# Kernel optimization log

Hardware: AMD Instinct MI355X
Metric: run time of the kernel (lower is better)

Reference implementation:

```python
import jax, jax.numpy as jnp
import numpy as np
from functools import partial

NUM_STEPS = 30  # Euler integration steps (inte_steps)


def _point_sample(vol, pts):
    """Trilinear sample of vol [C,D,H,W] at pts [N,3] (voxel coords, (d,h,w) order).
    Matches torch grid_sample(mode='bilinear', padding_mode='border', align_corners=True)
    after the normalize+flip done in PointPooling. Returns [C,N]."""
    dims = jnp.asarray(vol.shape[1:], dtype=pts.dtype)  # (D,H,W)
    p = jnp.clip(pts, 0.0, dims - 1.0)  # border padding == clamp coords
    p0 = jnp.floor(p)
    frac = p - p0  # [N,3]
    i0 = p0.astype(jnp.int32)
    i1 = jnp.minimum(i0 + 1, (dims - 1.0).astype(jnp.int32))
    d0, h0, w0 = i0[:, 0], i0[:, 1], i0[:, 2]
    d1, h1, w1 = i1[:, 0], i1[:, 1], i1[:, 2]
    fd, fh, fw = frac[:, 0], frac[:, 1], frac[:, 2]
    g = lambda d, h, w: vol[:, d, h, w]  # [C,N] gather
    c000, c001 = g(d0, h0, w0), g(d0, h0, w1)
    c010, c011 = g(d0, h1, w0), g(d0, h1, w1)
    c100, c101 = g(d1, h0, w0), g(d1, h0, w1)
    c110, c111 = g(d1, h1, w0), g(d1, h1, w1)
    c00 = c000 * (1 - fw) + c001 * fw
    c01 = c010 * (1 - fw) + c011 * fw
    c10 = c100 * (1 - fw) + c101 * fw
    c11 = c110 * (1 - fw) + c111 * fw
    c0 = c00 * (1 - fh) + c01 * fh
    c1 = c10 * (1 - fh) + c11 * fh
    return c0 * (1 - fd) + c1 * fd  # [C,N]


def _interp(flow, x):
    # flow [B,3,D,H,W], x [B,N,3] -> [B,N,3]
    out = jax.vmap(_point_sample)(flow, x)  # [B,3,N]
    return jnp.transpose(out, (0, 2, 1))


def _integrate_euler(flow, x, num_steps):
    flow = flow * (1.0 / num_steps)
    def step(x, _):
        return x + _interp(flow, x), None
    x, _ = jax.lax.scan(step, x, None, length=num_steps)
    return x


def _forward(verts, affine, flow_field):
    B, N, _ = verts.shape
    ones = jnp.ones((B, N, 1), dtype=verts.dtype)
    homog = jnp.concatenate([verts, ones], axis=-1)  # [B,N,4]
    pred = jnp.einsum('bij,bnj->bni', affine, homog)[..., :3]
    aux = _integrate_euler(flow_field, pred, NUM_STEPS)
    flow_int = aux - pred  # [B,N,3]
    pred = aux
    flow_int = jnp.transpose(flow_int, (0, 2, 1))[..., None, None]  # [B,3,N,1,1]
    homog2 = jnp.concatenate([pred, ones], axis=-1)
    inv_aff = jnp.linalg.inv(affine)
    pred = jnp.einsum('bij,bnj->bni', inv_aff, homog2)[..., :3]
    return pred, flow_int


def setup_inputs() -> dict:
    key = jax.random.key(0)
    k1, k2, k3 = jax.random.split(key, 3)
    B, N = 2, 140000
    D = H = W = 192
    dims = jnp.asarray([D - 1, H - 1, W - 1], dtype=jnp.float32)
    verts = jax.random.uniform(k1, (B, N, 3), dtype=jnp.float32) * dims
    affine = jnp.eye(4, dtype=jnp.float32)[None] + 0.01 * jax.random.normal(k2, (B, 4, 4), dtype=jnp.float32)
    flow_field = jax.random.normal(k3, (B, 3, D, H, W), dtype=jnp.float32)
    return {"verts": verts, "affine": affine, "flow_field": flow_field}


def reference(verts, affine, flow_field):
    return _forward(verts, affine, flow_field)
```

## Files before the change

### kernel.cpp

```cpp
#include <hip/hip_runtime.h>

#define NSTEPS 30
#define DIM 192
static constexpr int DHW = DIM * DIM * DIM;
static constexpr int PTS_PER_WAVE = 21;

__global__ void invert4x4_kernel(const float* __restrict__ aff,
                                 float* __restrict__ out, int B) {
    int b = blockIdx.x * blockDim.x + threadIdx.x;
    if (b >= B) return;
    double a[16];
#pragma unroll
    for (int i = 0; i < 16; i++) a[i] = (double)aff[b * 16 + i];

    double s0 = a[0]*a[5]  - a[4]*a[1];
    double s1 = a[0]*a[6]  - a[4]*a[2];
    double s2 = a[0]*a[7]  - a[4]*a[3];
    double s3 = a[1]*a[6]  - a[5]*a[2];
    double s4 = a[1]*a[7]  - a[5]*a[3];
    double s5 = a[2]*a[7]  - a[6]*a[3];
    double c5 = a[10]*a[15] - a[14]*a[11];
    double c4 = a[9]*a[15]  - a[13]*a[11];
    double c3 = a[9]*a[14]  - a[13]*a[10];
    double c2 = a[8]*a[15]  - a[12]*a[11];
    double c1 = a[8]*a[14]  - a[12]*a[10];
    double c0 = a[8]*a[13]  - a[12]*a[9];
    double det = s0*c5 - s1*c4 + s2*c3 + s3*c2 - s4*c1 + s5*c0;
    double inv = 1.0 / det;

    double o[16];
    o[0]  = ( a[5]*c5 - a[6]*c4 + a[7]*c3) * inv;
    o[1]  = (-a[1]*c5 + a[2]*c4 - a[3]*c3) * inv;
    o[2]  = ( a[13]*s5 - a[14]*s4 + a[15]*s3) * inv;
    o[3]  = (-a[9]*s5 + a[10]*s4 - a[11]*s3) * inv;
    o[4]  = (-a[4]*c5 + a[6]*c2 - a[7]*c1) * inv;
    o[5]  = ( a[0]*c5 - a[2]*c2 + a[3]*c1) * inv;
    o[6]  = (-a[12]*s5 + a[14]*s2 - a[15]*s1) * inv;
    o[7]  = ( a[8]*s5 - a[10]*s2 + a[11]*s1) * inv;
    o[8]  = ( a[4]*c4 - a[5]*c2 + a[7]*c0) * inv;
    o[9]  = (-a[0]*c4 + a[1]*c2 - a[3]*c0) * inv;
    o[10] = ( a[12]*s4 - a[13]*s2 + a[15]*s0) * inv;
    o[11] = (-a[8]*s4 + a[9]*s2 - a[11]*s0) * inv;
    o[12] = (-a[4]*c3 + a[5]*c1 - a[6]*c0) * inv;
    o[13] = ( a[0]*c3 - a[1]*c1 + a[2]*c0) * inv;
    o[14] = (-a[12]*s3 + a[13]*s1 - a[14]*s0) * inv;
    o[15] = ( a[8]*s3 - a[9]*s1 + a[10]*s0) * inv;
#pragma unroll
    for (int i = 0; i < 16; i++) out[b * 16 + i] = (float)o[i];
}

__global__ __launch_bounds__(256) void deform_kernel(
    const float* __restrict__ verts,
    const float* __restrict__ affine,
    const float* __restrict__ flow,
    const float* __restrict__ invaff,
    float* __restrict__ out_pred,
    float* __restrict__ out_flow,
    int N, int B) {
    int lane = threadIdx.x & 63;
    int wib  = threadIdx.x >> 6;
    long gwave = (long)blockIdx.x * (blockDim.x >> 6) + wib;

    int piw = lane / 3;
    if (piw > PTS_PER_WAVE - 1) piw = PTS_PER_WAVE - 1;
    int ch = lane - piw * 3;
    if (ch > 2) ch = 2;

    long pt = gwave * PTS_PER_WAVE + piw;
    bool valid = (lane < 63) && (pt < (long)B * N);
    long ptc = valid ? pt : ((long)B * N - 1);
    int b = (int)(ptc / N);
    int n = (int)(ptc - (long)b * N);

    const float* A = affine + b * 16;
    const float* v = verts + (size_t)ptc * 3;
    float vx = v[0], vy = v[1], vz = v[2];
    float x = A[0] * vx + A[1] * vy + A[2]  * vz + A[3];
    float y = A[4] * vx + A[5] * vy + A[6]  * vz + A[7];
    float z = A[8] * vx + A[9] * vy + A[10] * vz + A[11];
    float p0 = (ch == 0) ? x : (ch == 1) ? y : z;

    const float* Fc = flow + ((size_t)b * 3 + ch) * (size_t)DHW;
    const float scale = (float)(1.0 / NSTEPS);

    float cc[8];
    int key = -1;
    int bl = piw * 3;

    for (int s = 0; s < NSTEPS; s++) {
        float pd = fminf(fmaxf(x, 0.0f), (float)(DIM - 1));
        float ph = fminf(fmaxf(y, 0.0f), (float)(DIM - 1));
        float pw = fminf(fmaxf(z, 0.0f), (float)(DIM - 1));
        float fd0 = floorf(pd), fh0 = floorf(ph), fw0 = floorf(pw);
        int d0 = (int)fd0, h0 = (int)fh0, w0 = (int)fw0;
        float fd = pd - fd0, fh = ph - fh0, fw = pw - fw0;

        int k = (d0 * DIM + h0) * DIM + w0;
        if (k != key) {
            key = k;
            int d1 = min(d0 + 1, DIM - 1);
            int h1 = min(h0 + 1, DIM - 1);
            int w1 = min(w0 + 1, DIM - 1);
            int r00 = (d0 * DIM + h0) * DIM;
            int r01 = (d0 * DIM + h1) * DIM;
            int r10 = (d1 * DIM + h0) * DIM;
            int r11 = (d1 * DIM + h1) * DIM;
            cc[0] = Fc[r00 + w0] * scale;
            cc[1] = Fc[r00 + w1] * scale;
            cc[2] = Fc[r01 + w0] * scale;
            cc[3] = Fc[r01 + w1] * scale;
            cc[4] = Fc[r10 + w0] * scale;
            cc[5] = Fc[r10 + w1] * scale;
            cc[6] = Fc[r11 + w0] * scale;
            cc[7] = Fc[r11 + w1] * scale;
        }

        float omfw = 1.0f - fw, omfh = 1.0f - fh, omfd = 1.0f - fd;
        float c00 = cc[0] * omfw + cc[1] * fw;
        float c01 = cc[2] * omfw + cc[3] * fw;
        float c10 = cc[4] * omfw + cc[5] * fw;
        float c11 = cc[6] * omfw + cc[7] * fw;
        float c0 = c00 * omfh + c01 * fh;
        float c1 = c10 * omfh + c11 * fh;
        float val = c0 * omfd + c1 * fd;

        float v0 = __shfl(val, bl,     64);
        float v1 = __shfl(val, bl + 1, 64);
        float v2 = __shfl(val, bl + 2, 64);
        x += v0; y += v1; z += v2;
    }

    if (valid) {
        float posc = (ch == 0) ? x : (ch == 1) ? y : z;
        float fint = posc - p0;
        const float* Ai = invaff + b * 16 + ch * 4;
        float o = Ai[0] * x + Ai[1] * y + Ai[2] * z + Ai[3];
        out_pred[(size_t)ptc * 3 + ch] = o;
        out_flow[(size_t)b * 3 * N + (size_t)ch * N + n] = fint;
    }
}

extern "C" void kernel_launch(void* const* d_in, const int* in_sizes, int n_in,
                              void* d_out, int out_size, void* d_ws, size_t ws_size,
                              hipStream_t stream) {
    const float* verts  = (const float*)d_in[0];
    const float* affine = (const float*)d_in[1];
    const float* flow   = (const float*)d_in[2];

    int B = in_sizes[1] / 16;
    int N = in_sizes[0] / (3 * B);

    float* invaff   = (float*)d_ws;
    float* out_pred = (float*)d_out;
    float* out_flow = out_pred + (size_t)B * N * 3;

    hipLaunchKernelGGL(invert4x4_kernel, dim3(1), dim3(64), 0, stream,
                       affine, invaff, B);

    long total_pts = (long)B * N;
    long waves  = (total_pts + PTS_PER_WAVE - 1) / PTS_PER_WAVE;
    long blocks = (waves + 3) / 4;
    hipLaunchKernelGGL(deform_kernel, dim3((unsigned)blocks), dim3(256), 0, stream,
                       verts, affine, flow, invaff, out_pred, out_flow, N, B);
}
```

Baseline: 316.6 us.

## Repack flow field into interleaved fp16 channels before Euler integration

Result: faster. 306.1 us (-3.3%).

```diff
diff --git a/kernel.cpp b/kernel.cpp
--- a/kernel.cpp
+++ b/kernel.cpp
@@ -1,8 +1,9 @@
 #include <hip/hip_runtime.h>
+#include <hip/hip_fp16.h>
 
 #define NSTEPS 30
 #define DIM 192
-static constexpr int DHW = DIM * DIM * DIM;
+static constexpr long DHW = (long)DIM * DIM * DIM;
 static constexpr int PTS_PER_WAVE = 21;
 
 __global__ void invert4x4_kernel(const float* __restrict__ aff,
@@ -12,7 +13,6 @@
     double a[16];
 #pragma unroll
     for (int i = 0; i < 16; i++) a[i] = (double)aff[b * 16 + i];
-
     double s0 = a[0]*a[5]  - a[4]*a[1];
     double s1 = a[0]*a[6]  - a[4]*a[2];
     double s2 = a[0]*a[7]  - a[4]*a[3];
@@ -27,7 +27,6 @@
     double c0 = a[8]*a[13]  - a[12]*a[9];
     double det = s0*c5 - s1*c4 + s2*c3 + s3*c2 - s4*c1 + s5*c0;
     double inv = 1.0 / det;
-
     double o[16];
     o[0]  = ( a[5]*c5 - a[6]*c4 + a[7]*c3) * inv;
     o[1]  = (-a[1]*c5 + a[2]*c4 - a[3]*c3) * inv;
@@ -49,6 +48,113 @@
     for (int i = 0; i < 16; i++) out[b * 16 + i] = (float)o[i];
 }
 
+__global__ __launch_bounds__(256) void repack_kernel(const float* __restrict__ flow,
+                                                     __half* __restrict__ packed) {
+    long vox = (long)blockIdx.x * blockDim.x + threadIdx.x;
+    int b = blockIdx.y;
+    if (vox >= DHW) return;
+    const float* F = flow + (size_t)b * 3 * DHW;
+    float f0 = F[vox];
+    float f1 = F[vox + DHW];
+    float f2 = F[vox + 2 * DHW];
+    union { __half2 h2[2]; int2 i2; } u;
+    u.h2[0] = __floats2half2_rn(f0, f1);
+    u.h2[1] = __floats2half2_rn(f2, 0.0f);
+    reinterpret_cast<int2*>(packed)[(size_t)b * DHW + vox] = u.i2;
+}
+
+__global__ __launch_bounds__(256) void deform_packed_kernel(
+    const float* __restrict__ verts,
+    const float* __restrict__ affine,
+    const __half* __restrict__ packed,
+    const float* __restrict__ invaff,
+    float* __restrict__ out_pred,
+    float* __restrict__ out_flow,
+    int N, int B) {
+    int lane = threadIdx.x & 63;
+    int wib  = threadIdx.x >> 6;
+    long gwave = (long)blockIdx.x * (blockDim.x >> 6) + wib;
+
+    int piw = lane / 3;
+    if (piw > PTS_PER_WAVE - 1) piw = PTS_PER_WAVE - 1;
+    int ch = lane - piw * 3;
+    if (ch > 2) ch = 2;
+
+    long pt = gwave * PTS_PER_WAVE + piw;
+    bool valid = (lane < 63) && (pt < (long)B * N);
+    long ptc = valid ? pt : ((long)B * N - 1);
+    int b = (int)(ptc / N);
+    int n = (int)(ptc - (long)b * N);
+
+    const float* A = affine + b * 16;
+    const float* v = verts + (size_t)ptc * 3;
+    float vx = v[0], vy = v[1], vz = v[2];
+    float x = A[0] * vx + A[1] * vy + A[2]  * vz + A[3];
+    float y = A[4] * vx + A[5] * vy + A[6]  * vz + A[7];
+    float z = A[8] * vx + A[9] * vy + A[10] * vz + A[11];
+    float p0 = (ch == 0) ? x : (ch == 1) ? y : z;
+
+    const __half* Pb = packed + ((size_t)b * DHW) * 4 + ch;
+    const float scale = (float)(1.0 / NSTEPS);
+
+    float cc[8];
+    int key = -1;
+    int bl = piw * 3;
+
+    for (int s = 0; s < NSTEPS; s++) {
+        float pd = fminf(fmaxf(x, 0.0f), (float)(DIM - 1));
+        float ph = fminf(fmaxf(y, 0.0f), (float)(DIM - 1));
+        float pw = fminf(fmaxf(z, 0.0f), (float)(DIM - 1));
+        float fd0 = floorf(pd), fh0 = floorf(ph), fw0 = floorf(pw);
+        int d0 = (int)fd0, h0 = (int)fh0, w0 = (int)fw0;
+        float fd = pd - fd0, fh = ph - fh0, fw = pw - fw0;
+
+        int k = (d0 * DIM + h0) * DIM + w0;
+        if (k != key) {
+            key = k;
+            int d1 = min(d0 + 1, DIM - 1);
+            int h1 = min(h0 + 1, DIM - 1);
+            int w1 = min(w0 + 1, DIM - 1);
+            size_t r00 = (size_t)((d0 * DIM + h0) * DIM) * 4;
+            size_t r01 = (size_t)((d0 * DIM + h1) * DIM) * 4;
+            size_t r10 = (size_t)((d1 * DIM + h0) * DIM) * 4;
+            size_t r11 = (size_t)((d1 * DIM + h1) * DIM) * 4;
+            size_t o0 = (size_t)w0 * 4, o1 = (size_t)w1 * 4;
+            cc[0] = __half2float(Pb[r00 + o0]) * scale;
+            cc[1] = __half2float(Pb[r00 + o1]) * scale;
+            cc[2] = __half2float(Pb[r01 + o0]) * scale;
+            cc[3] = __half2float(Pb[r01 + o1]) * scale;
+            cc[4] = __half2float(Pb[r10 + o0]) * scale;
+            cc[5] = __half2float(Pb[r10 + o1]) * scale;
+            cc[6] = __half2float(Pb[r11 + o0]) * scale;
+            cc[7] = __half2float(Pb[r11 + o1]) * scale;
+        }
+
+        float omfw = 1.0f - fw, omfh = 1.0f - fh, omfd = 1.0f - fd;
+        float c00 = cc[0] * omfw + cc[1] * fw;
+        float c01 = cc[2] * omfw + cc[3] * fw;
+        float c10 = cc[4] * omfw + cc[5] * fw;
+        float c11 = cc[6] * omfw + cc[7] * fw;
+        float c0 = c00 * omfh + c01 * fh;
+        float c1 = c10 * omfh + c11 * fh;
+        float val = c0 * omfd + c1 * fd;
+
+        float v0 = __shfl(val, bl,     64);
+        float v1 = __shfl(val, bl + 1, 64);
+        float v2 = __shfl(val, bl + 2, 64);
+        x += v0; y += v1; z += v2;
+    }
+
+    if (valid) {
+        float posc = (ch == 0) ? x : (ch == 1) ? y : z;
+        float fint = posc - p0;
+        const float* Ai = invaff + b * 16 + ch * 4;
+        float o = Ai[0] * x + Ai[1] * y + Ai[2] * z + Ai[3];
+        out_pred[(size_t)ptc * 3 + ch] = o;
+        out_flow[(size_t)b * 3 * N + (size_t)ch * N + n] = fint;
+    }
+}
+
 __global__ __launch_bounds__(256) void deform_kernel(
     const float* __restrict__ verts,
     const float* __restrict__ affine,
@@ -60,18 +166,15 @@
     int lane = threadIdx.x & 63;
     int wib  = threadIdx.x >> 6;
     long gwave = (long)blockIdx.x * (blockDim.x >> 6) + wib;
-
     int piw = lane / 3;
     if (piw > PTS_PER_WAVE - 1) piw = PTS_PER_WAVE - 1;
     int ch = lane - piw * 3;
     if (ch > 2) ch = 2;
-
     long pt = gwave * PTS_PER_WAVE + piw;
     bool valid = (lane < 63) && (pt < (long)B * N);
     long ptc = valid ? pt : ((long)B * N - 1);
     int b = (int)(ptc / N);
     int n = (int)(ptc - (long)b * N);
-
     const float* A = affine + b * 16;
     const float* v = verts + (size_t)ptc * 3;
     float vx = v[0], vy = v[1], vz = v[2];
@@ -79,14 +182,11 @@
     float y = A[4] * vx + A[5] * vy + A[6]  * vz + A[7];
     float z = A[8] * vx + A[9] * vy + A[10] * vz + A[11];
     float p0 = (ch == 0) ? x : (ch == 1) ? y : z;
-
     const float* Fc = flow + ((size_t)b * 3 + ch) * (size_t)DHW;
     const float scale = (float)(1.0 / NSTEPS);
-
     float cc[8];
     int key = -1;
     int bl = piw * 3;
-
     for (int s = 0; s < NSTEPS; s++) {
         float pd = fminf(fmaxf(x, 0.0f), (float)(DIM - 1));
         float ph = fminf(fmaxf(y, 0.0f), (float)(DIM - 1));
@@ -94,7 +194,6 @@
         float fd0 = floorf(pd), fh0 = floorf(ph), fw0 = floorf(pw);
         int d0 = (int)fd0, h0 = (int)fh0, w0 = (int)fw0;
         float fd = pd - fd0, fh = ph - fh0, fw = pw - fw0;
-
         int k = (d0 * DIM + h0) * DIM + w0;
         if (k != key) {
             key = k;
@@ -114,7 +213,6 @@
             cc[6] = Fc[r11 + w0] * scale;
             cc[7] = Fc[r11 + w1] * scale;
         }
-
         float omfw = 1.0f - fw, omfh = 1.0f - fh, omfd = 1.0f - fd;
         float c00 = cc[0] * omfw + cc[1] * fw;
         float c01 = cc[2] * omfw + cc[3] * fw;
@@ -123,13 +221,11 @@
         float c0 = c00 * omfh + c01 * fh;
         float c1 = c10 * omfh + c11 * fh;
         float val = c0 * omfd + c1 * fd;
-
         float v0 = __shfl(val, bl,     64);
         float v1 = __shfl(val, bl + 1, 64);
         float v2 = __shfl(val, bl + 2, 64);
         x += v0; y += v1; z += v2;
     }
-
     if (valid) {
         float posc = (ch == 0) ? x : (ch == 1) ? y : z;
         float fint = posc - p0;
@@ -150,16 +246,33 @@
     int B = in_sizes[1] / 16;
     int N = in_sizes[0] / (3 * B);
 
-    float* invaff   = (float*)d_ws;
     float* out_pred = (float*)d_out;
     float* out_flow = out_pred + (size_t)B * N * 3;
 
-    hipLaunchKernelGGL(invert4x4_kernel, dim3(1), dim3(64), 0, stream,
-                       affine, invaff, B);
+    size_t packed_bytes = (size_t)B * DHW * 4 * sizeof(__half);
+    bool use_packed = (ws_size >= packed_bytes + 256);
 
     long total_pts = (long)B * N;
     long waves  = (total_pts + PTS_PER_WAVE - 1) / PTS_PER_WAVE;
     long blocks = (waves + 3) / 4;
-    hipLaunchKernelGGL(deform_kernel, dim3((unsigned)blocks), dim3(256), 0, stream,
-                       verts, affine, flow, invaff, out_pred, out_flow, N, B);
-}
+
+    if (use_packed) {
+        __half* packed = (__half*)d_ws;
+        float* invaff  = (float*)((char*)d_ws + packed_bytes);
+        hipLaunchKernelGGL(invert4x4_kernel, dim3(1), dim3(64), 0, stream,
+                           affine, invaff, B);
+        long vblocks = (DHW + 255) / 256;
+        hipLaunchKernelGGL(repack_kernel, dim3((unsigned)vblocks, B), dim3(256), 0,
+                           stream, flow, packed);
+        hipLaunchKernelGGL(deform_packed_kernel, dim3((unsigned)blocks), dim3(256),
+                           0, stream, verts, affine, packed, invaff,
+                           out_pred, out_flow, N, B);
+    } else {
+        float* invaff = (float*)d_ws;
+        hipLaunchKernelGGL(invert4x4_kernel, dim3(1), dim3(64), 0, stream,
+                           affine, invaff, B);
+        hipLaunchKernelGGL(deform_kernel, dim3((unsigned)blocks), dim3(256), 0,
+                           stream, verts, affine, flow, invaff,
+                           out_pred, out_flow, N, B);
+    }
+}
```

## Repack flow field into interleaved fp16 xyz layout and sample one point per thread

Applied to the files above, without the earlier changes.

After: 327.2 us. +3.3%, slower.

```diff
diff --git a/kernel.cpp b/kernel.cpp
--- a/kernel.cpp
+++ b/kernel.cpp
@@ -1,8 +1,9 @@
 #include <hip/hip_runtime.h>
+#include <hip/hip_fp16.h>
 
 #define NSTEPS 30
 #define DIM 192
-static constexpr int DHW = DIM * DIM * DIM;
+static constexpr long DHW = (long)DIM * DIM * DIM;
 static constexpr int PTS_PER_WAVE = 21;
 
 __global__ void invert4x4_kernel(const float* __restrict__ aff,
@@ -12,7 +13,6 @@
     double a[16];
 #pragma unroll
     for (int i = 0; i < 16; i++) a[i] = (double)aff[b * 16 + i];
-
     double s0 = a[0]*a[5]  - a[4]*a[1];
     double s1 = a[0]*a[6]  - a[4]*a[2];
     double s2 = a[0]*a[7]  - a[4]*a[3];
@@ -27,7 +27,6 @@
     double c0 = a[8]*a[13]  - a[12]*a[9];
     double det = s0*c5 - s1*c4 + s2*c3 + s3*c2 - s4*c1 + s5*c0;
     double inv = 1.0 / det;
-
     double o[16];
     o[0]  = ( a[5]*c5 - a[6]*c4 + a[7]*c3) * inv;
     o[1]  = (-a[1]*c5 + a[2]*c4 - a[3]*c3) * inv;
@@ -49,6 +48,135 @@
     for (int i = 0; i < 16; i++) out[b * 16 + i] = (float)o[i];
 }
 
+__global__ __launch_bounds__(256) void repack4_kernel(const float* __restrict__ flow,
+                                                      __half* __restrict__ packed) {
+    long q = (long)blockIdx.x * blockDim.x + threadIdx.x;
+    int b = blockIdx.y;
+    long v0 = q * 4;
+    if (v0 >= DHW) return;
+    const float* F = flow + (size_t)b * 3 * DHW;
+    float4 f0 = *reinterpret_cast<const float4*>(F + v0);
+    float4 f1 = *reinterpret_cast<const float4*>(F + v0 + DHW);
+    float4 f2 = *reinterpret_cast<const float4*>(F + v0 + 2 * DHW);
+    union { __half2 h[2]; int2 i2; } u;
+    int4 o0, o1;
+    u.h[0] = __floats2half2_rn(f0.x, f1.x); u.h[1] = __floats2half2_rn(f2.x, 0.f);
+    o0.x = u.i2.x; o0.y = u.i2.y;
+    u.h[0] = __floats2half2_rn(f0.y, f1.y); u.h[1] = __floats2half2_rn(f2.y, 0.f);
+    o0.z = u.i2.x; o0.w = u.i2.y;
+    u.h[0] = __floats2half2_rn(f0.z, f1.z); u.h[1] = __floats2half2_rn(f2.z, 0.f);
+    o1.x = u.i2.x; o1.y = u.i2.y;
+    u.h[0] = __floats2half2_rn(f0.w, f1.w); u.h[1] = __floats2half2_rn(f2.w, 0.f);
+    o1.z = u.i2.x; o1.w = u.i2.y;
+    int4* out = reinterpret_cast<int4*>(packed) + (((size_t)b * DHW + v0) >> 1);
+    out[0] = o0;
+    out[1] = o1;
+}
+
+static __device__ __forceinline__ float2 h2f(unsigned u) {
+    return __half22float2(__builtin_bit_cast(__half2, u));
+}
+
+__global__ __launch_bounds__(256) void deform1_kernel(
+    const float* __restrict__ verts,
+    const float* __restrict__ affine,
+    const __half* __restrict__ packed,
+    const float* __restrict__ invaff,
+    float* __restrict__ out_pred,
+    float* __restrict__ out_flow,
+    int N, int B) {
+    int idx = blockIdx.x * blockDim.x + threadIdx.x;
+    int total = B * N;
+    bool valid = idx < total;
+    int i = valid ? idx : total - 1;
+    int b = i / N;
+    int n = i - b * N;
+
+    const float* A = affine + b * 16;
+    const float* v = verts + (size_t)i * 3;
+    float vx = v[0], vy = v[1], vz = v[2];
+    float x = A[0] * vx + A[1] * vy + A[2]  * vz + A[3];
+    float y = A[4] * vx + A[5] * vy + A[6]  * vz + A[7];
+    float z = A[8] * vx + A[9] * vy + A[10] * vz + A[11];
+    const float px = x, py = y, pz = z;
+
+    const char* Pb = (const char*)(packed + (size_t)b * DHW * 4);
+    const float scale = (float)(1.0 / NSTEPS);
+
+    float cc[3][8];
+    int key = -1;
+
+    for (int s = 0; s < NSTEPS; s++) {
+        float pd = fminf(fmaxf(x, 0.0f), (float)(DIM - 1));
+        float ph = fminf(fmaxf(y, 0.0f), (float)(DIM - 1));
+        float pw = fminf(fmaxf(z, 0.0f), (float)(DIM - 1));
+        float fd0 = floorf(pd), fh0 = floorf(ph), fw0 = floorf(pw);
+        int d0 = (int)fd0, h0 = (int)fh0, w0 = (int)fw0;
+        float fd = pd - fd0, fh = ph - fh0, fw = pw - fw0;
+
+        int k = (d0 * DIM + h0) * DIM + w0;
+        if (k != key) {
+            key = k;
+            int d1 = min(d0 + 1, DIM - 1);
+            int h1 = min(h0 + 1, DIM - 1);
+            int lb = min(w0, DIM - 2);
+            int sel = w0 - lb;
+            int rr[4];
+            rr[0] = (d0 * DIM + h0) * DIM;
+            rr[1] = (d0 * DIM + h1) * DIM;
+            rr[2] = (d1 * DIM + h0) * DIM;
+            rr[3] = (d1 * DIM + h1) * DIM;
+#pragma unroll
+            for (int r = 0; r < 4; r++) {
+                const uint2* p = reinterpret_cast<const uint2*>(
+                    Pb + (size_t)(rr[r] + lb) * 8);
+                uint2 qa = p[0];
+                uint2 qb = p[1];
+                float2 a01 = h2f(qa.x), a2_ = h2f(qa.y);
+                float2 b01 = h2f(qb.x), b2_ = h2f(qb.y);
+                float c0a = sel ? b01.x : a01.x;
+                float c1a = sel ? b01.y : a01.y;
+                float c2a = sel ? b2_.x : a2_.x;
+                cc[0][2*r+0] = c0a  * scale; cc[0][2*r+1] = b01.x * scale;
+                cc[1][2*r+0] = c1a  * scale; cc[1][2*r+1] = b01.y * scale;
+                cc[2][2*r+0] = c2a  * scale; cc[2][2*r+1] = b2_.x * scale;
+            }
+        }
+
+        float omfw = 1.0f - fw, omfh = 1.0f - fh, omfd = 1.0f - fd;
+        float vals[3];
+#pragma unroll
+        for (int c = 0; c < 3; c++) {
+            float c00 = cc[c][0] * omfw + cc[c][1] * fw;
+            float c01 = cc[c][2] * omfw + cc[c][3] * fw;
+            float c10 = cc[c][4] * omfw + cc[c][5] * fw;
+            float c11 = cc[c][6] * omfw + cc[c][7] * fw;
+            float c0 = c00 * omfh + c01 * fh;
+            float c1 = c10 * omfh + c11 * fh;
+            vals[c] = c0 * omfd + c1 * fd;
+        }
+        x += vals[0];
+        y += vals[1];
+        z += vals[2];
+    }
+
+    if (valid) {
+        float fx = x - px, fy = y - py, fz = z - pz;
+        const float* Ai = invaff + b * 16;
+        float ox = Ai[0] * x + Ai[1] * y + Ai[2]  * z + Ai[3];
+        float oy = Ai[4] * x + Ai[5] * y + Ai[6]  * z + Ai[7];
+        float oz = Ai[8] * x + Ai[9] * y + Ai[10] * z + Ai[11];
+        size_t po = (size_t)i * 3;
+        out_pred[po + 0] = ox;
+        out_pred[po + 1] = oy;
+        out_pred[po + 2] = oz;
+        size_t fo = (size_t)b * 3 * N + n;
+        out_flow[fo]         = fx;
+        out_flow[fo + N]     = fy;
+        out_flow[fo + 2 * N] = fz;
+    }
+}
+
 __global__ __launch_bounds__(256) void deform_kernel(
     const float* __restrict__ verts,
     const float* __restrict__ affine,
@@ -60,18 +188,15 @@
     int lane = threadIdx.x & 63;
     int wib  = threadIdx.x >> 6;
     long gwave = (long)blockIdx.x * (blockDim.x >> 6) + wib;
-
     int piw = lane / 3;
     if (piw > PTS_PER_WAVE - 1) piw = PTS_PER_WAVE - 1;
     int ch = lane - piw * 3;
     if (ch > 2) ch = 2;
-
     long pt = gwave * PTS_PER_WAVE + piw;
     bool valid = (lane < 63) && (pt < (long)B * N);
     long ptc = valid ? pt : ((long)B * N - 1);
     int b = (int)(ptc / N);
     int n = (int)(ptc - (long)b * N);
-
     const float* A = affine + b * 16;
     const float* v = verts + (size_t)ptc * 3;
     float vx = v[0], vy = v[1], vz = v[2];
@@ -79,14 +204,11 @@
     float y = A[4] * vx + A[5] * vy + A[6]  * vz + A[7];
     float z = A[8] * vx + A[9] * vy + A[10] * vz + A[11];
     float p0 = (ch == 0) ? x : (ch == 1) ? y : z;
-
     const float* Fc = flow + ((size_t)b * 3 + ch) * (size_t)DHW;
     const float scale = (float)(1.0 / NSTEPS);
-
     float cc[8];
     int key = -1;
     int bl = piw * 3;
-
     for (int s = 0; s < NSTEPS; s++) {
         float pd = fminf(fmaxf(x, 0.0f), (float)(DIM - 1));
         float ph = fminf(fmaxf(y, 0.0f), (float)(DIM - 1));
@@ -94,7 +216,6 @@
         float fd0 = floorf(pd), fh0 = floorf(ph), fw0 = floorf(pw);
         int d0 = (int)fd0, h0 = (int)fh0, w0 = (int)fw0;
         float fd = pd - fd0, fh = ph - fh0, fw = pw - fw0;
-
         int k = (d0 * DIM + h0) * DIM + w0;
         if (k != key) {
             key = k;
@@ -114,7 +235,6 @@
             cc[6] = Fc[r11 + w0] * scale;
             cc[7] = Fc[r11 + w1] * scale;
         }
-
         float omfw = 1.0f - fw, omfh = 1.0f - fh, omfd = 1.0f - fd;
         float c00 = cc[0] * omfw + cc[1] * fw;
         float c01 = cc[2] * omfw + cc[3] * fw;
@@ -123,13 +243,11 @@
         float c0 = c00 * omfh + c01 * fh;
         float c1 = c10 * omfh + c11 * fh;
         float val = c0 * omfd + c1 * fd;
-
         float v0 = __shfl(val, bl,     64);
         float v1 = __shfl(val, bl + 1, 64);
         float v2 = __shfl(val, bl + 2, 64);
         x += v0; y += v1; z += v2;
     }
-
     if (valid) {
         float posc = (ch == 0) ? x : (ch == 1) ? y : z;
         float fint = posc - p0;
@@ -150,16 +268,34 @@
     int B = in_sizes[1] / 16;
     int N = in_sizes[0] / (3 * B);
 
-    float* invaff   = (float*)d_ws;
     float* out_pred = (float*)d_out;
     float* out_flow = out_pred + (size_t)B * N * 3;
 
-    hipLaunchKernelGGL(invert4x4_kernel, dim3(1), dim3(64), 0, stream,
-                       affine, invaff, B);
-
-    long total_pts = (long)B * N;
-    long waves  = (total_pts + PTS_PER_WAVE - 1) / PTS_PER_WAVE;
-    long blocks = (waves + 3) / 4;
-    hipLaunchKernelGGL(deform_kernel, dim3((unsigned)blocks), dim3(256), 0, stream,
-                       verts, affine, flow, invaff, out_pred, out_flow, N, B);
-}
+    size_t packed_bytes = (size_t)B * DHW * 4 * sizeof(__half);
+    bool use_packed = (ws_size >= packed_bytes + 256);
+
+    int total = B * N;
+
+    if (use_packed) {
+        __half* packed = (__half*)d_ws;
+        float* invaff  = (float*)((char*)d_ws + packed_bytes);
+        hipLaunchKernelGGL(invert4x4_kernel, dim3(1), dim3(64), 0, stream,
+                           affine, invaff, B);
+        long quads = (DHW + 3) / 4;
+        long vblocks = (quads + 255) / 256;
+        hipLaunchKernelGGL(repack4_kernel, dim3((unsigned)vblocks, B), dim3(256), 0,
+                           stream, flow, packed);
+        int blocks = (total + 255) / 256;
+        hipLaunchKernelGGL(deform1_kernel, dim3(blocks), dim3(256), 0, stream,
+                           verts, affine, packed, invaff, out_pred, out_flow, N, B);
+    } else {
+        float* invaff = (float*)d_ws;
+        hipLaunchKernelGGL(invert4x4_kernel, dim3(1), dim3(64), 0, stream,
+                           affine, invaff, B);
+        long waves  = ((long)total + PTS_PER_WAVE - 1) / PTS_PER_WAVE;
+        long blocks = (waves + 3) / 4;
+        hipLaunchKernelGGL(deform_kernel, dim3((unsigned)blocks), dim3(256), 0,
+                           stream, verts, affine, flow, invaff,
+                           out_pred, out_flow, N, B);
+    }
+}
```
